# Performance work log

Measured on AMD Instinct MI355X. Metric: run time of the kernel, lower is better.

## Reference

```python
import jax, jax.numpy as jnp
import numpy as np

CHANNELS = 128
HEADS = 4
R = 2
LAMBDA = 0.1


def setup_inputs() -> dict:
    key = jax.random.key(0)
    k1, k2 = jax.random.split(key)
    x = jax.random.normal(k1, (1, CHANNELS, 32, 32, 32), dtype=jnp.float32)
    # 1x1x1 Conv3d weight [3C, C] (trailing unit spatial dims dropped), fan-in scaled
    w_qkv = jax.random.normal(k2, (3 * CHANNELS, CHANNELS), dtype=jnp.float32) * (CHANNELS ** -0.5)
    return {"x": x, "w_qkv": w_qkv}


def reference(x, w_qkv):
    head_dim = CHANNELS // HEADS          # 32
    d_half = head_dim // 2                # 16
    scale = head_dim ** -0.5
    # AvgPool3d(kernel_size=1, stride=R) == strided subsampling
    xs = x[:, :, ::R, ::R, ::R]
    B, C, H, W, Z = xs.shape
    N = H * W * Z                          # 4096 tokens
    # 1x1x1 conv == pointwise channel matmul, then group channels heads-major
    qkv = jnp.einsum('oc,bchwz->bohwz', w_qkv, xs).reshape(B, HEADS, 3 * head_dim, N)
    q, k, v = jnp.split(qkv, 3, axis=2)    # each [B, h, head_dim, N]
    q1, q2 = q[:, :, :d_half, :], q[:, :, d_half:, :]
    k1, k2 = k[:, :, :d_half, :], k[:, :, d_half:, :]
    # two full score matrices [B, h, N, N] (differential attention)
    attn1 = jnp.einsum('bhdn,bhdm->bhnm', q1, k1) * scale
    attn2 = jnp.einsum('bhdn,bhdm->bhnm', q2, k2) * scale
    diff_attn = jax.nn.softmax(attn1, axis=-1) - LAMBDA * jax.nn.softmax(attn2, axis=-1)
    out = jnp.einsum('bhnm,bhdm->bhnd', diff_attn, v)  # [B, h, N, head_dim]
    # faithful to torch .view(B, -1, H, W, Z) on contiguous (h, N, head_dim) layout
    return out.reshape(B, C, H, W, Z)
```

## Files before the change

### kernel.cpp

```cpp
#include <hip/hip_runtime.h>

#define N_TOK 4096
#define NH    4

typedef __attribute__((ext_vector_type(8))) short bf16x8;
typedef __attribute__((ext_vector_type(4))) short bf16x4;
typedef __attribute__((ext_vector_type(4))) float f32x4;

static constexpr float SCALE   = 0.17677669529663687f;
static constexpr float QSCALE  = 0.25503632254435463f;
static constexpr float LAMBDA_ = 0.1f;
#define PSTRIDE 2112

__device__ __forceinline__ unsigned short bf_rne(float f) {
    unsigned u = __float_as_uint(f);
    u += 0x7FFF + ((u >> 16) & 1);
    return (unsigned short)(u >> 16);
}

__device__ __forceinline__ void async_copy16(const unsigned short* g, unsigned short* l) {
    __builtin_amdgcn_global_load_lds(
        (const __attribute__((address_space(1))) void*)g,
        (__attribute__((address_space(3))) void*)l, 16, 0, 0);
}

__global__ __launch_bounds__(256) void prep_w_kernel(
    const float* __restrict__ w,
    unsigned short* __restrict__ wh, unsigned short* __restrict__ wl)
{
    int idx = blockIdx.x * 256 + threadIdx.x;
    int row = idx >> 7;
    int rr  = row % 96;
    float sc = (rr < 32) ? QSCALE : 1.0f;
    float f  = w[idx] * sc;
    unsigned u = __float_as_uint(f);
    float lo = f - __uint_as_float(u & 0xFFFF0000u);
    wh[idx] = (unsigned short)(u >> 16);
    wl[idx] = (unsigned short)(__float_as_uint(lo) >> 16);
}

__global__ __launch_bounds__(256) void qkv_kernel(
    const float* __restrict__ x,
    const unsigned short* __restrict__ wh, const unsigned short* __restrict__ wl,
    unsigned short* __restrict__ qA, unsigned short* __restrict__ kB,
    unsigned short* __restrict__ vT)
{
    __shared__ __align__(16) float xf[16][132];
    __shared__ __align__(16) unsigned short xbh[16 * 136];
    __shared__ __align__(16) unsigned short xbl[16 * 136];
    __shared__ __align__(16) unsigned short qsh[2][16][64];
    __shared__ __align__(16) unsigned short ksh[2][16][64];
    __shared__ __align__(16) unsigned short vsh[2][32][16];

    const int t  = threadIdx.x;
    const int tg = blockIdx.x >> 1;
    const int rh = blockIdx.x & 1;
    const int n0 = tg * 16;
    const int nh = n0 >> 8, nw = (n0 >> 4) & 15;
    const int xbase = nh * 2048 + nw * 64;

    #pragma unroll
    for (int k = 0; k < 8; ++k) {
        int idx = t + k * 256;
        int tok = idx & 15, ch = idx >> 4;
        xf[tok][ch] = x[(size_t)ch * 32768 + xbase + tok * 2];
    }
    __syncthreads();
    #pragma unroll
    for (int k = 0; k < 8; ++k) {
        int idx = t + k * 256;
        int tok = idx & 15, ch = idx >> 4;
        float f = xf[tok][ch];
        unsigned u = __float_as_uint(f);
        float lo = f - __uint_as_float(u & 0xFFFF0000u);
        xbh[tok * 136 + ch] = (unsigned short)(u >> 16);
        xbl[tok * 136 + ch] = (unsigned short)(__float_as_uint(lo) >> 16);
    }
    __syncthreads();

    const int lane = t & 63;
    const int m    = lane & 15;
    const int quad = lane >> 4;
    const int w    = t >> 6;

    bf16x8 Bh[4], Bl[4];
    #pragma unroll
    for (int s = 0; s < 4; ++s) {
        Bh[s] = *(const bf16x8*)&xbh[m * 136 + s * 32 + quad * 8];
        Bl[s] = *(const bf16x8*)&xbl[m * 136 + s * 32 + quad * 8];
    }

    #pragma unroll
    for (int rt = 0; rt < 3; ++rt) {
        const int R0 = rh * 192 + w * 48 + rt * 16;
        const unsigned short* whp = wh + (size_t)(R0 + m) * 128;
        const unsigned short* wlp = wl + (size_t)(R0 + m) * 128;
        bf16x8 Ah[4], Al[4];
        #pragma unroll
        for (int s = 0; s < 4; ++s) {
            Ah[s] = *(const bf16x8*)(whp + s * 32 + quad * 8);
            Al[s] = *(const bf16x8*)(wlp + s * 32 + quad * 8);
        }
        f32x4 C = {0, 0, 0, 0};
        #pragma unroll
        for (int s = 0; s < 4; ++s) {
            C = __builtin_amdgcn_mfma_f32_16x16x32_bf16(Ah[s], Bh[s], C, 0, 0, 0);
            C = __builtin_amdgcn_mfma_f32_16x16x32_bf16(Al[s], Bh[s], C, 0, 0, 0);
            C = __builtin_amdgcn_mfma_f32_16x16x32_bf16(Ah[s], Bl[s], C, 0, 0, 0);
        }
        #pragma unroll
        for (int i = 0; i < 4; ++i) {
            int R  = R0 + quad * 4 + i;
            int hh = R / 96;
            int rr = R - hh * 96;
            int hl = hh & 1;
            float f = C[i];
            if (rr < 64) {
                unsigned u = __float_as_uint(f);
                float lo = f - __uint_as_float(u & 0xFFFF0000u);
                unsigned short hi16 = (unsigned short)(u >> 16);
                unsigned short lo16 = (unsigned short)(__float_as_uint(lo) >> 16);
                int part = (rr & 31) >> 4, d = rr & 15;
                if (rr < 32) {
                    qsh[hl][m][part * 32 + d]      = hi16;
                    qsh[hl][m][part * 32 + d + 16] = lo16;
                } else {
                    ksh[hl][m][part * 32 + d]      = hi16;
                    ksh[hl][m][part * 32 + d + 16] = lo16;
                }
            } else {
                vsh[hl][rr - 64][m] = bf_rne(f);
            }
        }
    }
    __syncthreads();

    {
        int rec = t >> 3, ch8 = t & 7;
        int hl  = rec >> 4, i = rec & 15;
        int hh  = rh * 2 + hl;
        size_t base = ((size_t)hh * N_TOK + n0 + i) * 64 + ch8 * 8;
        *(uint4*)(qA + base) = *(const uint4*)&qsh[hl][i][ch8 * 8];
        *(uint4*)(kB + base) = *(const uint4*)&ksh[hl][i][ch8 * 8];
    }
    if (t < 128) {
        int hl = t >> 6, d = (t >> 1) & 31, half = t & 1;
        int hh = rh * 2 + hl;
        int kb = (n0 >> 3) + half;
        *(uint4*)(vT + (size_t)hh * 131072 + kb * 256 + d * 8) =
            *(const uint4*)&vsh[hl][d][half * 8];
    }
}

__global__ __launch_bounds__(256, 4) void flash_kernel(
    const unsigned short* __restrict__ qA, const unsigned short* __restrict__ kB,
    const unsigned short* __restrict__ vT, float* __restrict__ parts)
{
    __shared__ __align__(16) unsigned short kv_sh[2][6144];
    __shared__ float Obuf[2][2][16][32];
    __shared__ float lbuf[2][2][16];

    const int t    = threadIdx.x;
    const int w    = t >> 6;
    const int lane = t & 63;
    const int m    = lane & 15;
    const int quad = lane >> 4;
    const int ks   = blockIdx.x & 1;
    const int qt   = (blockIdx.x >> 1) & 127;
    const int h    = blockIdx.x >> 8;
    const int qtile = w >> 1;
    const int kh    = w & 1;
    const int qbase = qt * 32;

    const unsigned short* kBh = kB + (size_t)h * N_TOK * 64;
    const unsigned short* vTh = vT + (size_t)h * 131072;
    const int key0 = ks * 2048;

    auto stage = [&](int tile, int b) {
        const unsigned short* kben = kBh + (size_t)(key0 + tile * 64) * 64;
        const unsigned short* vben = vTh + (size_t)((key0 >> 3) + tile * 8) * 256;
        #pragma unroll
        for (int i = 0; i < 3; ++i) {
            int s = i * 256 + t;
            const unsigned short* src;
            if (s < 512) {
                int ml = s >> 3, p = s & 7, c = p ^ (ml & 7);
                src = kben + ml * 64 + c * 8;
            } else {
                int s2 = s - 512;
                int kb_l = s2 >> 5, d = s2 & 31;
                src = vben + kb_l * 256 + d * 8;
            }
            async_copy16(src, &kv_sh[b][s * 8]);
        }
    };

    stage(0, 0);

    for (int i = t; i < 2048; i += 256) ((float*)Obuf)[i] = 0.f;
    if (t < 64) ((float*)lbuf)[t] = 0.f;

    const unsigned short* qrec = qA + (size_t)(h * N_TOK + qbase + qtile * 16 + m) * 64;
    const bf16x8 zz = {0,0,0,0,0,0,0,0};
    bf16x8 Bq1h = *(const bf16x8*)(qrec + (quad & 1) * 8);
    bf16x8 Bq2h = *(const bf16x8*)(qrec + 32 + (quad & 1) * 8);
    bf16x8 Bq1l = (quad < 2) ? *(const bf16x8*)(qrec + 16 + quad * 8) : zz;
    bf16x8 Bq2l = (quad < 2) ? *(const bf16x8*)(qrec + 48 + quad * 8) : zz;

    f32x4 O1a = {0,0,0,0}, O1b = {0,0,0,0}, O2a = {0,0,0,0}, O2b = {0,0,0,0};
    float l1 = 0.f, l2 = 0.f;

    const int ml0 = kh * 32 + m, ml1 = ml0 + 16;
    const int a1o0 = ml0 * 64 + ((quad)     ^ (ml0 & 7)) * 8;
    const int a2o0 = ml0 * 64 + ((4 + quad) ^ (ml0 & 7)) * 8;
    const int a1o1 = ml1 * 64 + ((quad)     ^ (ml1 & 7)) * 8;
    const int a2o1 = ml1 * 64 + ((4 + quad) ^ (ml1 & 7)) * 8;
    const int kbl0 = kh * 4 + (quad >> 1);
    const int v0o0 = 4096 + (kbl0 * 32 + m)      * 8 + (quad & 1) * 4;
    const int v1o0 = 4096 + (kbl0 * 32 + 16 + m) * 8 + (quad & 1) * 4;
    const int v0o1 = v0o0 + 512;
    const int v1o1 = v1o0 + 512;

    for (int tile = 0; tile < 32; ++tile) {
        const int b = tile & 1;
        __syncthreads();
        if (tile + 1 < 32) stage(tile + 1, b ^ 1);

        const unsigned short* buf = kv_sh[b];
        bf16x8 K1_0 = *(const bf16x8*)(buf + a1o0);
        bf16x8 K2_0 = *(const bf16x8*)(buf + a2o0);
        bf16x8 K1_1 = *(const bf16x8*)(buf + a1o1);
        bf16x8 K2_1 = *(const bf16x8*)(buf + a2o1);

        f32x4 sA1 = {0,0,0,0}, sA2 = {0,0,0,0};
        f32x4 sB1 = {0,0,0,0}, sB2 = {0,0,0,0};
        sA1 = __builtin_amdgcn_mfma_f32_16x16x32_bf16(K1_0, Bq1h, sA1, 0, 0, 0);
        sB1 = __builtin_amdgcn_mfma_f32_16x16x32_bf16(K1_1, Bq1h, sB1, 0, 0, 0);
        sA1 = __builtin_amdgcn_mfma_f32_16x16x32_bf16(K1_0, Bq1l, sA1, 0, 0, 0);
        sB1 = __builtin_amdgcn_mfma_f32_16x16x32_bf16(K1_1, Bq1l, sB1, 0, 0, 0);
        sA2 = __builtin_amdgcn_mfma_f32_16x16x32_bf16(K2_0, Bq2h, sA2, 0, 0, 0);
        sB2 = __builtin_amdgcn_mfma_f32_16x16x32_bf16(K2_1, Bq2h, sB2, 0, 0, 0);
        sA2 = __builtin_amdgcn_mfma_f32_16x16x32_bf16(K2_0, Bq2l, sA2, 0, 0, 0);
        sB2 = __builtin_amdgcn_mfma_f32_16x16x32_bf16(K2_1, Bq2l, sB2, 0, 0, 0);

        float pa0 = __builtin_amdgcn_exp2f(sA1[0]), pa1 = __builtin_amdgcn_exp2f(sA1[1]);
        float pa2 = __builtin_amdgcn_exp2f(sA1[2]), pa3 = __builtin_amdgcn_exp2f(sA1[3]);
        float pb0 = __builtin_amdgcn_exp2f(sB1[0]), pb1 = __builtin_amdgcn_exp2f(sB1[1]);
        float pb2 = __builtin_amdgcn_exp2f(sB1[2]), pb3 = __builtin_amdgcn_exp2f(sB1[3]);
        float qa0 = __builtin_amdgcn_exp2f(sA2[0]), qa1 = __builtin_amdgcn_exp2f(sA2[1]);
        float qa2 = __builtin_amdgcn_exp2f(sA2[2]), qa3 = __builtin_amdgcn_exp2f(sA2[3]);
        float qb0 = __builtin_amdgcn_exp2f(sB2[0]), qb1 = __builtin_amdgcn_exp2f(sB2[1]);
        float qb2 = __builtin_amdgcn_exp2f(sB2[2]), qb3 = __builtin_amdgcn_exp2f(sB2[3]);
        l1 += (pa0 + pa1) + (pa2 + pa3) + (pb0 + pb1) + (pb2 + pb3);
        l2 += (qa0 + qa1) + (qa2 + qa3) + (qb0 + qb1) + (qb2 + qb3);
        union { unsigned u[2]; bf16x4 v; } cA1, cB1, cA2, cB2;
        cA1.u[0] = __builtin_amdgcn_perm(__float_as_uint(pa1), __float_as_uint(pa0), 0x07060302u);
        cA1.u[1] = __builtin_amdgcn_perm(__float_as_uint(pa3), __float_as_uint(pa2), 0x07060302u);
        cB1.u[0] = __builtin_amdgcn_perm(__float_as_uint(pb1), __float_as_uint(pb0), 0x07060302u);
        cB1.u[1] = __builtin_amdgcn_perm(__float_as_uint(pb3), __float_as_uint(pb2), 0x07060302u);
        cA2.u[0] = __builtin_amdgcn_perm(__float_as_uint(qa1), __float_as_uint(qa0), 0x07060302u);
        cA2.u[1] = __builtin_amdgcn_perm(__float_as_uint(qa3), __float_as_uint(qa2), 0x07060302u);
        cB2.u[0] = __builtin_amdgcn_perm(__float_as_uint(qb1), __float_as_uint(qb0), 0x07060302u);
        cB2.u[1] = __builtin_amdgcn_perm(__float_as_uint(qb3), __float_as_uint(qb2), 0x07060302u);

        bf16x4 V00 = *(const bf16x4*)(buf + v0o0);
        bf16x4 V10 = *(const bf16x4*)(buf + v1o0);
        bf16x4 V01 = *(const bf16x4*)(buf + v0o1);
        bf16x4 V11 = *(const bf16x4*)(buf + v1o1);

        O1a = __builtin_amdgcn_mfma_f32_16x16x16bf16_1k(cA1.v, V00, O1a, 0, 0, 0);
        O1b = __builtin_amdgcn_mfma_f32_16x16x16bf16_1k(cA1.v, V10, O1b, 0, 0, 0);
        O2a = __builtin_amdgcn_mfma_f32_16x16x16bf16_1k(cA2.v, V00, O2a, 0, 0, 0);
        O2b = __builtin_amdgcn_mfma_f32_16x16x16bf16_1k(cA2.v, V10, O2b, 0, 0, 0);
        O1a = __builtin_amdgcn_mfma_f32_16x16x16bf16_1k(cB1.v, V01, O1a, 0, 0, 0);
        O1b = __builtin_amdgcn_mfma_f32_16x16x16bf16_1k(cB1.v, V11, O1b, 0, 0, 0);
        O2a = __builtin_amdgcn_mfma_f32_16x16x16bf16_1k(cB2.v, V01, O2a, 0, 0, 0);
        O2b = __builtin_amdgcn_mfma_f32_16x16x16bf16_1k(cB2.v, V11, O2b, 0, 0, 0);
    }

    l1 += __shfl_xor(l1, 16, 64); l1 += __shfl_xor(l1, 32, 64);
    l2 += __shfl_xor(l2, 16, 64); l2 += __shfl_xor(l2, 32, 64);
    if (lane < 16) {
        atomicAdd(&lbuf[qtile][0][m], l1);
        atomicAdd(&lbuf[qtile][1][m], l2);
    }
    #pragma unroll
    for (int i = 0; i < 4; ++i) {
        int r = quad * 4 + i;
        atomicAdd(&Obuf[qtile][0][r][m],      O1a[i]);
        atomicAdd(&Obuf[qtile][0][r][16 + m], O1b[i]);
        atomicAdd(&Obuf[qtile][1][r][m],      O2a[i]);
        atomicAdd(&Obuf[qtile][1][r][16 + m], O2b[i]);
    }
    __syncthreads();

    float* dst = parts + (size_t)((h * 128 + qt) * 2 + ks) * PSTRIDE;
    for (int i = t; i < 1024; i += 256) {
        int r = i >> 5, d = i & 31;
        int qtl = r >> 4, rl = r & 15;
        dst[i]        = Obuf[qtl][0][rl][d];
        dst[1024 + i] = Obuf[qtl][1][rl][d];
    }
    if (t < 32) {
        int qtl = t >> 4, rl = t & 15;
        dst[2048 + t] = lbuf[qtl][0][rl];
        dst[2080 + t] = lbuf[qtl][1][rl];
    }
}

__global__ __launch_bounds__(256) void merge_kernel(
    const float* __restrict__ parts, float* __restrict__ out)
{
    int idx = blockIdx.x * 256 + threadIdx.x;
    int row = idx >> 5, d = idx & 31;
    int h = row >> 12, n = row & 4095;
    int qt = n >> 5, r = n & 31;
    const float* p0 = parts + (size_t)((h * 128 + qt) * 2) * PSTRIDE;
    const float* p1 = p0 + PSTRIDE;
    float o1 = p0[r * 32 + d]        + p1[r * 32 + d];
    float o2 = p0[1024 + r * 32 + d] + p1[1024 + r * 32 + d];
    float l1 = p0[2048 + r]          + p1[2048 + r];
    float l2 = p0[2080 + r]          + p1[2080 + r];
    out[idx] = o1 / l1 - LAMBDA_ * o2 / l2;
}

extern "C" void kernel_launch(void* const* d_in, const int* in_sizes, int n_in,
                              void* d_out, int out_size, void* d_ws, size_t ws_size,
                              hipStream_t stream) {
    const float* x = (const float*)d_in[0];
    const float* w = (const float*)d_in[1];
    float* out = (float*)d_out;

    unsigned short* qA = (unsigned short*)d_ws;
    unsigned short* kB = qA + (size_t)NH * N_TOK * 64;
    unsigned short* vT = kB + (size_t)NH * N_TOK * 64;
    float* parts = (float*)(vT + (size_t)NH * 32 * N_TOK);
    unsigned short* wh = (unsigned short*)(parts + (size_t)1024 * PSTRIDE);
    unsigned short* wl = wh + 384 * 128;

    prep_w_kernel<<<192, 256, 0, stream>>>(w, wh, wl);
    qkv_kernel<<<512, 256, 0, stream>>>(x, wh, wl, qA, kB, vT);
    flash_kernel<<<1024, 256, 0, stream>>>(qA, kB, vT, parts);
    merge_kernel<<<2048, 256, 0, stream>>>(parts, out);
}
```

Measured before the change: 134.2 us.

## Fuse weight prep into qkv kernel and merge into flash via tickets

Drops the separate weight-split kernel: each qkv block now loads fp32 weights, scales them and splits them into bf16 hi/lo in registers. Drops the separate merge kernel: after a flash block writes its partial, it bumps a per-query-tile atomic ticket, and whichever of the two key-split blocks finishes second combines both partials and writes the output. Ticket counters are zeroed by block 0 of the qkv kernel. This removes two kernel launches and the extra pass over the partials, at the cost of redundant weight conversion in every qkv block plus threadfence and atomic overhead.

New measurement: 269.8 us. +101.1%, slower.

```diff
diff --git a/kernel.cpp b/kernel.cpp
--- a/kernel.cpp
+++ b/kernel.cpp
@@ -24,26 +24,14 @@
         (__attribute__((address_space(3))) void*)l, 16, 0, 0);
 }
 
-__global__ __launch_bounds__(256) void prep_w_kernel(
-    const float* __restrict__ w,
-    unsigned short* __restrict__ wh, unsigned short* __restrict__ wl)
-{
-    int idx = blockIdx.x * 256 + threadIdx.x;
-    int row = idx >> 7;
-    int rr  = row % 96;
-    float sc = (rr < 32) ? QSCALE : 1.0f;
-    float f  = w[idx] * sc;
-    unsigned u = __float_as_uint(f);
-    float lo = f - __uint_as_float(u & 0xFFFF0000u);
-    wh[idx] = (unsigned short)(u >> 16);
-    wl[idx] = (unsigned short)(__float_as_uint(lo) >> 16);
+__device__ __forceinline__ unsigned pack_hi(float a, float b) {
+    return __builtin_amdgcn_perm(__float_as_uint(b), __float_as_uint(a), 0x07060302u);
 }
 
 __global__ __launch_bounds__(256) void qkv_kernel(
-    const float* __restrict__ x,
-    const unsigned short* __restrict__ wh, const unsigned short* __restrict__ wl,
+    const float* __restrict__ x, const float* __restrict__ w,
     unsigned short* __restrict__ qA, unsigned short* __restrict__ kB,
-    unsigned short* __restrict__ vT)
+    unsigned short* __restrict__ vT, unsigned* __restrict__ tickets)
 {
     __shared__ __align__(16) float xf[16][132];
     __shared__ __align__(16) unsigned short xbh[16 * 136];
@@ -56,8 +44,13 @@
     const int tg = blockIdx.x >> 1;
     const int rh = blockIdx.x & 1;
     const int n0 = tg * 16;
-    const int nh = n0 >> 8, nw = (n0 >> 4) & 15;
-    const int xbase = nh * 2048 + nw * 64;
+    const int nhh = n0 >> 8, nw = (n0 >> 4) & 15;
+    const int xbase = nhh * 2048 + nw * 64;
+
+    if (blockIdx.x == 0) {
+        tickets[t] = 0u;
+        tickets[t + 256] = 0u;
+    }
 
     #pragma unroll
     for (int k = 0; k < 8; ++k) {
@@ -81,7 +74,7 @@
     const int lane = t & 63;
     const int m    = lane & 15;
     const int quad = lane >> 4;
-    const int w    = t >> 6;
+    const int wv   = t >> 6;
 
     bf16x8 Bh[4], Bl[4];
     #pragma unroll
@@ -92,14 +85,30 @@
 
     #pragma unroll
     for (int rt = 0; rt < 3; ++rt) {
-        const int R0 = rh * 192 + w * 48 + rt * 16;
-        const unsigned short* whp = wh + (size_t)(R0 + m) * 128;
-        const unsigned short* wlp = wl + (size_t)(R0 + m) * 128;
+        const int R0 = rh * 192 + wv * 48 + rt * 16;
+        const float sq = ((R0 % 96) < 32) ? QSCALE : 1.0f;
+        const float* wp = w + (size_t)(R0 + m) * 128;
         bf16x8 Ah[4], Al[4];
         #pragma unroll
         for (int s = 0; s < 4; ++s) {
-            Ah[s] = *(const bf16x8*)(whp + s * 32 + quad * 8);
-            Al[s] = *(const bf16x8*)(wlp + s * 32 + quad * 8);
+            float4 wa = *(const float4*)(wp + s * 32 + quad * 8);
+            float4 wb = *(const float4*)(wp + s * 32 + quad * 8 + 4);
+            float f0 = wa.x * sq, f1 = wa.y * sq, f2 = wa.z * sq, f3 = wa.w * sq;
+            float f4 = wb.x * sq, f5 = wb.y * sq, f6 = wb.z * sq, f7 = wb.w * sq;
+            float g0 = f0 - __uint_as_float(__float_as_uint(f0) & 0xFFFF0000u);
+            float g1 = f1 - __uint_as_float(__float_as_uint(f1) & 0xFFFF0000u);
+            float g2 = f2 - __uint_as_float(__float_as_uint(f2) & 0xFFFF0000u);
+            float g3 = f3 - __uint_as_float(__float_as_uint(f3) & 0xFFFF0000u);
+            float g4 = f4 - __uint_as_float(__float_as_uint(f4) & 0xFFFF0000u);
+            float g5 = f5 - __uint_as_float(__float_as_uint(f5) & 0xFFFF0000u);
+            float g6 = f6 - __uint_as_float(__float_as_uint(f6) & 0xFFFF0000u);
+            float g7 = f7 - __uint_as_float(__float_as_uint(f7) & 0xFFFF0000u);
+            union { unsigned u[4]; bf16x8 v; } ah, al;
+            ah.u[0] = pack_hi(f0, f1); ah.u[1] = pack_hi(f2, f3);
+            ah.u[2] = pack_hi(f4, f5); ah.u[3] = pack_hi(f6, f7);
+            al.u[0] = pack_hi(g0, g1); al.u[1] = pack_hi(g2, g3);
+            al.u[2] = pack_hi(g4, g5); al.u[3] = pack_hi(g6, g7);
+            Ah[s] = ah.v; Al[s] = al.v;
         }
         f32x4 C = {0, 0, 0, 0};
         #pragma unroll
@@ -154,11 +163,13 @@
 
 __global__ __launch_bounds__(256, 4) void flash_kernel(
     const unsigned short* __restrict__ qA, const unsigned short* __restrict__ kB,
-    const unsigned short* __restrict__ vT, float* __restrict__ parts)
+    const unsigned short* __restrict__ vT, float* __restrict__ parts,
+    unsigned* __restrict__ tickets, float* __restrict__ out)
 {
     __shared__ __align__(16) unsigned short kv_sh[2][6144];
     __shared__ float Obuf[2][2][16][32];
     __shared__ float lbuf[2][2][16];
+    __shared__ unsigned done_flag;
 
     const int t    = threadIdx.x;
     const int w    = t >> 6;
@@ -254,14 +265,10 @@
         l1 += (pa0 + pa1) + (pa2 + pa3) + (pb0 + pb1) + (pb2 + pb3);
         l2 += (qa0 + qa1) + (qa2 + qa3) + (qb0 + qb1) + (qb2 + qb3);
         union { unsigned u[2]; bf16x4 v; } cA1, cB1, cA2, cB2;
-        cA1.u[0] = __builtin_amdgcn_perm(__float_as_uint(pa1), __float_as_uint(pa0), 0x07060302u);
-        cA1.u[1] = __builtin_amdgcn_perm(__float_as_uint(pa3), __float_as_uint(pa2), 0x07060302u);
-        cB1.u[0] = __builtin_amdgcn_perm(__float_as_uint(pb1), __float_as_uint(pb0), 0x07060302u);
-        cB1.u[1] = __builtin_amdgcn_perm(__float_as_uint(pb3), __float_as_uint(pb2), 0x07060302u);
-        cA2.u[0] = __builtin_amdgcn_perm(__float_as_uint(qa1), __float_as_uint(qa0), 0x07060302u);
-        cA2.u[1] = __builtin_amdgcn_perm(__float_as_uint(qa3), __float_as_uint(qa2), 0x07060302u);
-        cB2.u[0] = __builtin_amdgcn_perm(__float_as_uint(qb1), __float_as_uint(qb0), 0x07060302u);
-        cB2.u[1] = __builtin_amdgcn_perm(__float_as_uint(qb3), __float_as_uint(qb2), 0x07060302u);
+        cA1.u[0] = pack_hi(pa0, pa1); cA1.u[1] = pack_hi(pa2, pa3);
+        cB1.u[0] = pack_hi(pb0, pb1); cB1.u[1] = pack_hi(pb2, pb3);
+        cA2.u[0] = pack_hi(qa0, qa1); cA2.u[1] = pack_hi(qa2, qa3);
+        cB2.u[0] = pack_hi(qb0, qb1); cB2.u[1] = pack_hi(qb2, qb3);
 
         bf16x4 V00 = *(const bf16x4*)(buf + v0o0);
         bf16x4 V10 = *(const bf16x4*)(buf + v1o0);
@@ -306,22 +313,25 @@
         dst[2048 + t] = lbuf[qtl][0][rl];
         dst[2080 + t] = lbuf[qtl][1][rl];
     }
-}
-
-__global__ __launch_bounds__(256) void merge_kernel(
-    const float* __restrict__ parts, float* __restrict__ out)
-{
-    int idx = blockIdx.x * 256 + threadIdx.x;
-    int row = idx >> 5, d = idx & 31;
-    int h = row >> 12, n = row & 4095;
-    int qt = n >> 5, r = n & 31;
-    const float* p0 = parts + (size_t)((h * 128 + qt) * 2) * PSTRIDE;
-    const float* p1 = p0 + PSTRIDE;
-    float o1 = p0[r * 32 + d]        + p1[r * 32 + d];
-    float o2 = p0[1024 + r * 32 + d] + p1[1024 + r * 32 + d];
-    float l1 = p0[2048 + r]          + p1[2048 + r];
-    float l2 = p0[2080 + r]          + p1[2080 + r];
-    out[idx] = o1 / l1 - LAMBDA_ * o2 / l2;
+
+    __threadfence();
+    __syncthreads();
+    if (t == 0) done_flag = atomicAdd(&tickets[h * 128 + qt], 1u);
+    __syncthreads();
+    if (done_flag == 1u) {
+        __threadfence();
+        const float* p0 = parts + (size_t)((h * 128 + qt) * 2) * PSTRIDE;
+        const float* p1 = p0 + PSTRIDE;
+        float* ob = out + (size_t)(h * N_TOK + qbase) * 32;
+        for (int i = t; i < 1024; i += 256) {
+            int r = i >> 5, d = i & 31;
+            float o1  = p0[r * 32 + d]        + p1[r * 32 + d];
+            float o2  = p0[1024 + r * 32 + d] + p1[1024 + r * 32 + d];
+            float l1v = p0[2048 + r]          + p1[2048 + r];
+            float l2v = p0[2080 + r]          + p1[2080 + r];
+            ob[i] = o1 / l1v - LAMBDA_ * o2 / l2v;
+        }
+    }
 }
 
 extern "C" void kernel_launch(void* const* d_in, const int* in_sizes, int n_in,
@@ -335,11 +345,8 @@
     unsigned short* kB = qA + (size_t)NH * N_TOK * 64;
     unsigned short* vT = kB + (size_t)NH * N_TOK * 64;
     float* parts = (float*)(vT + (size_t)NH * 32 * N_TOK);
-    unsigned short* wh = (unsigned short*)(parts + (size_t)1024 * PSTRIDE);
-    unsigned short* wl = wh + 384 * 128;
-
-    prep_w_kernel<<<192, 256, 0, stream>>>(w, wh, wl);
-    qkv_kernel<<<512, 256, 0, stream>>>(x, wh, wl, qA, kB, vT);
-    flash_kernel<<<1024, 256, 0, stream>>>(qA, kB, vT, parts);
-    merge_kernel<<<2048, 256, 0, stream>>>(parts, out);
-}
+    unsigned* tickets = (unsigned*)(parts + (size_t)1024 * PSTRIDE);
+
+    qkv_kernel<<<512, 256, 0, stream>>>(x, w, qA, kB, vT, tickets);
+    flash_kernel<<<1024, 256, 0, stream>>>(qA, kB, vT, parts, tickets, out);
+}
```
